# Kernel tuning notes

Hardware: AMD Instinct MI355X
Metric: run time of the kernel (lower is better)

## Reference

```python
import jax, jax.numpy as jnp
import numpy as np

B, L, D = 128, 64, 1024  # batch, tokens, encoder_size
T = 2 * L - 1            # L shifts then L-1 reduces (full binary parse)


def setup_inputs() -> dict:
    key = jax.random.key(0)
    k1, k2, k3, k4 = jax.random.split(key, 4)
    sequence = jax.random.normal(k1, (B, L, 2 * D), dtype=jnp.float32)
    # valid SPINN transition sequence: shift all tokens, then reduce to one node
    transitions = jnp.concatenate(
        [jnp.ones((B, L), jnp.int32), jnp.full((B, L - 1), 2, jnp.int32)], axis=1)
    scale = 0.02
    Ul_w = jax.random.normal(k2, (D, 5 * D), dtype=jnp.float32) * scale  # U_l weight (x @ W)
    Ul_b = jax.random.normal(k3, (5 * D,), dtype=jnp.float32) * scale    # U_l bias
    Ur_w = jax.random.normal(k4, (D, 5 * D), dtype=jnp.float32) * scale  # U_r weight (no bias)
    return {"sequence": sequence, "transitions": transitions,
            "Ul_w": Ul_w, "Ul_b": Ul_b, "Ur_w": Ur_w}


def reference(sequence, transitions, Ul_w, Ul_b, Ur_w):
    b, l, d2 = sequence.shape
    d = d2 // 2
    seq_h, seq_c = sequence[..., :d], sequence[..., d:]
    S = l + 2  # max stack depth: 2 initial copies + l shifts
    batch = jnp.arange(b)

    # stack initialized with two copies of the first buffer token (buffer NOT popped)
    stack_h = jnp.zeros((b, S, d), seq_h.dtype).at[:, 0].set(seq_h[:, 0]).at[:, 1].set(seq_h[:, 0])
    stack_c = jnp.zeros((b, S, d), seq_c.dtype).at[:, 0].set(seq_c[:, 0]).at[:, 1].set(seq_c[:, 0])
    sp = jnp.full((b,), 2, jnp.int32)   # stack pointer (next free slot)
    bp = jnp.zeros((b,), jnp.int32)     # buffer pointer (next token to shift)

    def step(carry, trans):
        stack_h, stack_c, sp, bp = carry
        is_shift = trans == 1
        is_reduce = trans == 2
        # top-2 of stack: right = top, left = second
        h_r = stack_h[batch, sp - 1]
        c_r = stack_c[batch, sp - 1]
        h_l = stack_h[batch, sp - 2]
        c_l = stack_c[batch, sp - 2]
        # TreeLSTM composition (tracking input x is None)
        gates = h_l @ Ul_w + Ul_b + h_r @ Ur_w  # (b, 5d)
        i_j, o_j, f_l, f_r, u_j = jnp.split(gates, 5, axis=1)
        c_j = (jax.nn.sigmoid(i_j) * jnp.tanh(u_j)
               + jax.nn.sigmoid(f_l) * c_l + jax.nn.sigmoid(f_r) * c_r)
        h_j = jax.nn.sigmoid(o_j) * jnp.tanh(c_j)
        # buffer head for shift
        buf_h = seq_h[batch, bp]
        buf_c = seq_c[batch, bp]
        # single conditional scatter: shift writes at sp, reduce overwrites sp-2
        widx = jnp.where(is_shift, sp, sp - 2)
        cur_h = stack_h[batch, widx]
        cur_c = stack_c[batch, widx]
        sm = is_shift[:, None]
        rm = is_reduce[:, None]
        new_h = jnp.where(sm, buf_h, jnp.where(rm, h_j, cur_h))
        new_c = jnp.where(sm, buf_c, jnp.where(rm, c_j, cur_c))
        stack_h = stack_h.at[batch, widx].set(new_h)
        stack_c = stack_c.at[batch, widx].set(new_c)
        sp = sp + jnp.where(is_shift, 1, jnp.where(is_reduce, -1, 0)).astype(sp.dtype)
        bp = bp + is_shift.astype(bp.dtype)
        return (stack_h, stack_c, sp, bp), None

    (stack_h, _, sp, _), _ = jax.lax.scan(step, (stack_h, stack_c, sp, bp), transitions.T)
    return stack_h[batch, sp - 1]  # (B, D) final hidden state on top of each stack
```

## Files before the change

kernel.cpp:

```cpp
#include <hip/hip_runtime.h>
#include <hip/hip_bf16.h>


#define ND 5120
#define NSTEP 63
#define RHS (128 * 1024)
#define NBLK2 256

typedef __attribute__((ext_vector_type(8))) short bf16x8;
typedef __attribute__((ext_vector_type(4))) float f32x4;
typedef unsigned short u16;
typedef unsigned int u32;

__device__ __forceinline__ float bf2f(u16 x) {
  unsigned int u = ((unsigned int)x) << 16;
  return __builtin_bit_cast(float, u);
}
__device__ __forceinline__ u16 f2bf(float f) {
  unsigned int u = __builtin_bit_cast(unsigned int, f);
  unsigned int lsb = (u >> 16) & 1u;
  u += 0x7fffu + lsb;
  return (u16)(u >> 16);
}
__device__ __forceinline__ void gld16(const void* g, void* l) {
  __builtin_amdgcn_global_load_lds((const __attribute__((address_space(1))) void*)g,
                                   (__attribute__((address_space(3))) void*)l, 16, 0, 0);
}

__global__ void transpose_cast_kernel(const float* __restrict__ W, u16* __restrict__ WT) {
  __shared__ float tile[64][65];
  int bid = blockIdx.x;
  int kt = bid & 15, nt = bid >> 4;
  int tid = threadIdx.x;
#pragma unroll
  for (int i = 0; i < 16; ++i) {
    int idx = i * 256 + tid;
    int r = idx >> 6, c = idx & 63;
    tile[r][c] = W[(long)(kt * 64 + r) * ND + nt * 64 + c];
  }
  __syncthreads();
#pragma unroll
  for (int i = 0; i < 16; ++i) {
    int idx = i * 256 + tid;
    int r = idx >> 6, c = idx & 63;
    WT[(long)(nt * 64 + r) * 1024 + kt * 64 + c] = f2bf(tile[c][r]);
  }
}

__global__ void prep_misc_kernel(const float* __restrict__ seq, u16* __restrict__ Xh,
                                 u16* __restrict__ RH0, float* __restrict__ RC0,
                                 int* __restrict__ bar) {
  long t = (long)blockIdx.x * 256 + threadIdx.x;
  int idx = (int)(t >> 17);
  int rem = (int)(t & 131071);
  int b = rem >> 10;
  int k = rem & 1023;
  float h = seq[((long)b * 64 + idx) * 2048 + k];
  Xh[t] = f2bf(h);
  if (idx == 63) {
    RH0[rem] = f2bf(h);
    RC0[rem] = seq[((long)b * 64 + 63) * 2048 + 1024 + k];
  }
  if (t < 2048) bar[t] = 0;
}

__launch_bounds__(256)
__global__ void phase1_kernel(const u16* __restrict__ Xh, const u16* __restrict__ WlT,
                              const float* __restrict__ Ulb, u16* __restrict__ GL) {
  __shared__ u16 As[128 * 32];
  __shared__ u16 Bs[128 * 32];
  int bid = blockIdx.x;
  int mi = bid & 63, ni = bid >> 6;
  int t = threadIdx.x;
  int w = t >> 6, lane = t & 63;
  int r16 = lane & 15, quad = lane >> 4;
  int wm = w & 1, wn = w >> 1;
  const long arow0 = (long)mi * 128;
  const long brow0 = (long)ni * 128;
  int srow = 16 * w + (lane >> 2);
  int skoff = (lane & 3) * 8;

  f32x4 acc[4][4];
#pragma unroll
  for (int a = 0; a < 4; ++a)
#pragma unroll
    for (int b = 0; b < 4; ++b) acc[a][b] = (f32x4){0.f, 0.f, 0.f, 0.f};

  for (int ks = 0; ks < 32; ++ks) {
    long k0 = (long)ks * 32 + skoff;
    gld16(Xh + (arow0 + srow) * 1024 + k0,        As + w * 512);
    gld16(Xh + (arow0 + 64 + srow) * 1024 + k0,   As + 2048 + w * 512);
    gld16(WlT + (brow0 + srow) * 1024 + k0,       Bs + w * 512);
    gld16(WlT + (brow0 + 64 + srow) * 1024 + k0,  Bs + 2048 + w * 512);
    __syncthreads();
    bf16x8 af[4], bf[4];
#pragma unroll
    for (int mt = 0; mt < 4; ++mt)
      af[mt] = *(const bf16x8*)(As + (wm * 64 + mt * 16 + r16) * 32 + quad * 8);
#pragma unroll
    for (int nt = 0; nt < 4; ++nt)
      bf[nt] = *(const bf16x8*)(Bs + (wn * 64 + nt * 16 + r16) * 32 + quad * 8);
#pragma unroll
    for (int mt = 0; mt < 4; ++mt)
#pragma unroll
      for (int nt = 0; nt < 4; ++nt)
        acc[mt][nt] = __builtin_amdgcn_mfma_f32_16x16x32_bf16(af[mt], bf[nt], acc[mt][nt], 0, 0, 0);
    __syncthreads();
  }
#pragma unroll
  for (int mt = 0; mt < 4; ++mt)
#pragma unroll
    for (int nt = 0; nt < 4; ++nt)
#pragma unroll
      for (int r = 0; r < 4; ++r) {
        long row = arow0 + wm * 64 + mt * 16 + quad * 4 + r;
        long col = brow0 + wn * 64 + nt * 16 + r16;
        GL[row * ND + col] = f2bf(acc[mt][nt][r] + Ulb[col]);
      }
}

__device__ __forceinline__ void group_barrier(int* __restrict__ bar, int grp, int cg) {
  __syncthreads();
  if (threadIdx.x == 0) {
    asm volatile("s_waitcnt vmcnt(0)" ::: "memory");
    int* base = bar + grp * 320;
    int* gen = base + 9 * 32;
    int g0 = __hip_atomic_load(gen, __ATOMIC_RELAXED, __HIP_MEMORY_SCOPE_AGENT);
    int sub = cg & 7;
    int a = __hip_atomic_fetch_add(base + sub * 32, 1, __ATOMIC_RELAXED, __HIP_MEMORY_SCOPE_AGENT);
    if (a == 7) {
      __hip_atomic_fetch_add(base + sub * 32, -8, __ATOMIC_RELAXED, __HIP_MEMORY_SCOPE_AGENT);
      int m = __hip_atomic_fetch_add(base + 8 * 32, 1, __ATOMIC_RELAXED, __HIP_MEMORY_SCOPE_AGENT);
      if (m == 7) {
        __hip_atomic_fetch_add(base + 8 * 32, -8, __ATOMIC_RELAXED, __HIP_MEMORY_SCOPE_AGENT);
        __hip_atomic_fetch_add(gen, 1, __ATOMIC_RELAXED, __HIP_MEMORY_SCOPE_AGENT);
      } else {
        while (__hip_atomic_load(gen, __ATOMIC_RELAXED, __HIP_MEMORY_SCOPE_AGENT) == g0)
          __builtin_amdgcn_s_sleep(2);
      }
    } else {
      while (__hip_atomic_load(gen, __ATOMIC_RELAXED, __HIP_MEMORY_SCOPE_AGENT) == g0)
        __builtin_amdgcn_s_sleep(2);
    }
    __atomic_signal_fence(__ATOMIC_ACQUIRE);
  }
  __syncthreads();
}

__launch_bounds__(512, 1)
__global__ void phase2_kernel(const float* __restrict__ seq, const u16* __restrict__ WrT,
                              const u16* __restrict__ GL, const u16* __restrict__ RH0,
                              u16* __restrict__ Xring, const float* __restrict__ RC0,
                              int* __restrict__ bar, float* __restrict__ out) {
  __shared__ float plds[4][5][32][18];
  int bid = blockIdx.x;
  int rhf = bid & 3, cg = bid >> 2;
  int tid = threadIdx.x;
  int wv = tid >> 6, lane = tid & 63;
  int r16 = lane & 15, quad = lane >> 4;
  int mt = wv & 1, kq = wv >> 1;
  int col = cg * 16 + r16;
  int rowA = rhf * 32 + mt * 16;
  int kbase = kq * 256 + quad * 8;

  bf16x8 bw[5][8];
#pragma unroll
  for (int g = 0; g < 5; ++g)
#pragma unroll
    for (int ks = 0; ks < 8; ++ks)
      bw[g][ks] = *(const bf16x8*)(WrT + (long)(g * 1024 + col) * 1024 + kbase + ks * 32);
#pragma unroll
  for (int g = 0; g < 5; ++g)
#pragma unroll
    for (int ks = 0; ks < 8; ++ks)
      asm volatile("" : "+v"(bw[g][ks]));

  const long aoff = (long)(rowA + r16) * 1024 + kbase;

  int act = tid < 256;
  int row_l = tid >> 3, cp = tid & 7;
  int erow = rhf * 32 + row_l;
  int ecol0 = cg * 16 + cp * 2;
  float c0 = 0.f, c1 = 0.f;
  if (act) {
    c0 = RC0[(long)erow * 1024 + ecol0];
    c1 = RC0[(long)erow * 1024 + ecol0 + 1];
  }

  for (int j = 1; j <= NSTEP; ++j) {
    const u16* rhbuf = (j == 1) ? RH0 : (Xring + (long)(j - 2) * RHS);
    int idx = 63 - j;

    bf16x8 af[8];
#pragma unroll
    for (int ks = 0; ks < 8; ++ks)
      af[ks] = *(const bf16x8*)(rhbuf + aoff + ks * 32);
    u32 pgl[5];
    float2 pcl = {0.f, 0.f};
    if (act) {
      long glb = ((long)idx * 128 + erow) * ND + ecol0;
#pragma unroll
      for (int g = 0; g < 5; ++g)
        pgl[g] = *(const u32*)(GL + glb + g * 1024);
      pcl = *(const float2*)(seq + ((long)erow * 64 + idx) * 2048 + 1024 + ecol0);
    }

    f32x4 acc[5];
#pragma unroll
    for (int g = 0; g < 5; ++g) acc[g] = (f32x4){0.f, 0.f, 0.f, 0.f};
#pragma unroll
    for (int ks = 0; ks < 8; ++ks)
#pragma unroll
      for (int g = 0; g < 5; ++g)
        acc[g] = __builtin_amdgcn_mfma_f32_16x16x32_bf16(af[ks], bw[g][ks], acc[g], 0, 0, 0);

#pragma unroll
    for (int g = 0; g < 5; ++g)
#pragma unroll
      for (int r = 0; r < 4; ++r)
        plds[kq][g][mt * 16 + quad * 4 + r][r16] = acc[g][r];
    __syncthreads();

    if (act) {
      float h0, h1;
#pragma unroll
      for (int c = 0; c < 2; ++c) {
        int cl = cp * 2 + c;
        float gg[5];
#pragma unroll
        for (int g = 0; g < 5; ++g)
          gg[g] = plds[0][g][row_l][cl] + plds[1][g][row_l][cl] +
                  plds[2][g][row_l][cl] + plds[3][g][row_l][cl];
        u16 glo = (c == 0) ? 0 : 0;
        float gi  = gg[0] + bf2f((u16)((c ? pgl[0] >> 16 : pgl[0]) & 0xffff));
        float go  = gg[1] + bf2f((u16)((c ? pgl[1] >> 16 : pgl[1]) & 0xffff));
        float gfl = gg[2] + bf2f((u16)((c ? pgl[2] >> 16 : pgl[2]) & 0xffff));
        float gfr = gg[3] + bf2f((u16)((c ? pgl[3] >> 16 : pgl[3]) & 0xffff));
        float gu  = gg[4] + bf2f((u16)((c ? pgl[4] >> 16 : pgl[4]) & 0xffff));
        float c_l = c ? pcl.y : pcl.x;
        float c_r = c ? c1 : c0;
        float si  = 1.f / (1.f + __expf(-gi));
        float so  = 1.f / (1.f + __expf(-go));
        float sfl = 1.f / (1.f + __expf(-gfl));
        float sfr = 1.f / (1.f + __expf(-gfr));
        float cj = si * tanhf(gu) + sfl * c_l + sfr * c_r;
        float hj = so * tanhf(cj);
        if (c == 0) { c0 = cj; h0 = hj; } else { c1 = cj; h1 = hj; }
        (void)glo;
      }
      if (j < NSTEP) {
        u32 hv = (u32)f2bf(h0) | ((u32)f2bf(h1) << 16);
        u32* dst = (u32*)Xring + (long)(j - 1) * (RHS / 2) + erow * 512 + cg * 8 + cp;
        __hip_atomic_store(dst, hv, __ATOMIC_RELAXED, __HIP_MEMORY_SCOPE_AGENT);
      } else {
        float2 o2 = {h0, h1};
        *(float2*)(out + (long)erow * 1024 + ecol0) = o2;
      }
    }
    if (j < NSTEP) group_barrier(bar, rhf, cg);
  }
}

extern "C" void kernel_launch(void* const* d_in, const int* in_sizes, int n_in,
                              void* d_out, int out_size, void* d_ws, size_t ws_size,
                              hipStream_t stream) {
  const float* seq = (const float*)d_in[0];
  const float* Ulw = (const float*)d_in[2];
  const float* Ulb = (const float*)d_in[3];
  const float* Urw = (const float*)d_in[4];
  float* out = (float*)d_out;

  char* p = (char*)d_ws;
  u16* WlT = (u16*)p;  p += 10485760;
  u16* WrT = (u16*)p;  p += 10485760;
  u16* Xh  = (u16*)p;  p += 16777216;
  u16* GL  = (u16*)p;  p += 83886080;
  u16* RH0 = (u16*)p;  p += 524288;
  float* RC0 = (float*)p; p += 1048576;
  int* bar = (int*)p;  p += 8192;

  hipLaunchKernelGGL(transpose_cast_kernel, dim3(1280), dim3(256), 0, stream, Ulw, WlT);
  hipLaunchKernelGGL(transpose_cast_kernel, dim3(1280), dim3(256), 0, stream, Urw, WrT);
  hipLaunchKernelGGL(prep_misc_kernel, dim3(32768), dim3(256), 0, stream, seq, Xh, RH0, RC0, bar);
  hipLaunchKernelGGL(phase1_kernel, dim3(2560), dim3(256), 0, stream, Xh, WlT, Ulb, GL);
  hipLaunchKernelGGL(phase2_kernel, dim3(NBLK2), dim3(512), 0, stream,
                     seq, WrT, GL, RH0, Xh, RC0, bar, out);
}
```

Measured before the change: 566.9 us.

## Replace group barrier with per-wave readiness flags in recurrent phase

Removes the hierarchical atomic group barrier between recurrence steps. Each producing wave now publishes a flag once its hidden-state slice is stored, and each consumer wave spins only on the flags covering its own K-slice of the next step's input. The goal is to cut barrier latency and let waves run ahead as soon as their inputs are ready. In exchange, the per-step __syncthreads that protected shared-memory partials from being overwritten is gone, so there is a possible intra-block race. A bounded spin loop that can exit on timeout also risks silently reading stale data.

```diff
diff --git a/kernel.cpp b/kernel.cpp
--- a/kernel.cpp
+++ b/kernel.cpp
@@ -49,7 +49,7 @@
 
 __global__ void prep_misc_kernel(const float* __restrict__ seq, u16* __restrict__ Xh,
                                  u16* __restrict__ RH0, float* __restrict__ RC0,
-                                 int* __restrict__ bar) {
+                                 int* __restrict__ flags) {
   long t = (long)blockIdx.x * 256 + threadIdx.x;
   int idx = (int)(t >> 17);
   int rem = (int)(t & 131071);
@@ -61,7 +61,7 @@
     RH0[rem] = f2bf(h);
     RC0[rem] = seq[((long)b * 64 + 63) * 2048 + 1024 + k];
   }
-  if (t < 2048) bar[t] = 0;
+  if (t < 63488) flags[t] = 0;
 }
 
 __launch_bounds__(256)
@@ -119,39 +119,11 @@
       }
 }
 
-__device__ __forceinline__ void group_barrier(int* __restrict__ bar, int grp, int cg) {
-  __syncthreads();
-  if (threadIdx.x == 0) {
-    asm volatile("s_waitcnt vmcnt(0)" ::: "memory");
-    int* base = bar + grp * 320;
-    int* gen = base + 9 * 32;
-    int g0 = __hip_atomic_load(gen, __ATOMIC_RELAXED, __HIP_MEMORY_SCOPE_AGENT);
-    int sub = cg & 7;
-    int a = __hip_atomic_fetch_add(base + sub * 32, 1, __ATOMIC_RELAXED, __HIP_MEMORY_SCOPE_AGENT);
-    if (a == 7) {
-      __hip_atomic_fetch_add(base + sub * 32, -8, __ATOMIC_RELAXED, __HIP_MEMORY_SCOPE_AGENT);
-      int m = __hip_atomic_fetch_add(base + 8 * 32, 1, __ATOMIC_RELAXED, __HIP_MEMORY_SCOPE_AGENT);
-      if (m == 7) {
-        __hip_atomic_fetch_add(base + 8 * 32, -8, __ATOMIC_RELAXED, __HIP_MEMORY_SCOPE_AGENT);
-        __hip_atomic_fetch_add(gen, 1, __ATOMIC_RELAXED, __HIP_MEMORY_SCOPE_AGENT);
-      } else {
-        while (__hip_atomic_load(gen, __ATOMIC_RELAXED, __HIP_MEMORY_SCOPE_AGENT) == g0)
-          __builtin_amdgcn_s_sleep(2);
-      }
-    } else {
-      while (__hip_atomic_load(gen, __ATOMIC_RELAXED, __HIP_MEMORY_SCOPE_AGENT) == g0)
-        __builtin_amdgcn_s_sleep(2);
-    }
-    __atomic_signal_fence(__ATOMIC_ACQUIRE);
-  }
-  __syncthreads();
-}
-
 __launch_bounds__(512, 1)
 __global__ void phase2_kernel(const float* __restrict__ seq, const u16* __restrict__ WrT,
                               const u16* __restrict__ GL, const u16* __restrict__ RH0,
                               u16* __restrict__ Xring, const float* __restrict__ RC0,
-                              int* __restrict__ bar, float* __restrict__ out) {
+                              int* __restrict__ flags, float* __restrict__ out) {
   __shared__ float plds[4][5][32][18];
   int bid = blockIdx.x;
   int rhf = bid & 3, cg = bid >> 2;
@@ -187,14 +159,11 @@
     c1 = RC0[(long)erow * 1024 + ecol0 + 1];
   }
 
+  int* const gflags = flags;
+
   for (int j = 1; j <= NSTEP; ++j) {
-    const u16* rhbuf = (j == 1) ? RH0 : (Xring + (long)(j - 2) * RHS);
-    int idx = 63 - j;
-
-    bf16x8 af[8];
-#pragma unroll
-    for (int ks = 0; ks < 8; ++ks)
-      af[ks] = *(const bf16x8*)(rhbuf + aoff + ks * 32);
+    const int idx = 63 - j;
+
     u32 pgl[5];
     float2 pcl = {0.f, 0.f};
     if (act) {
@@ -205,6 +174,24 @@
       pcl = *(const float2*)(seq + ((long)erow * 64 + idx) * 2048 + 1024 + ecol0);
     }
 
+    if (j >= 2) {
+      const int fbase = ((rhf * 62 + (j - 2)) * 64 + kq * 16) * 4 + lane;
+      int spin = 0;
+      for (;;) {
+        int v = __hip_atomic_load(gflags + fbase, __ATOMIC_RELAXED, __HIP_MEMORY_SCOPE_AGENT);
+        if (__all(v != 0)) break;
+        if (++spin > (1 << 17)) break;
+        __builtin_amdgcn_s_sleep(1);
+      }
+      asm volatile("" ::: "memory");
+    }
+
+    const u16* rhbuf = (j == 1) ? RH0 : (Xring + (long)(j - 2) * RHS);
+    bf16x8 af[8];
+#pragma unroll
+    for (int ks = 0; ks < 8; ++ks)
+      af[ks] = *(const bf16x8*)(rhbuf + aoff + ks * 32);
+
     f32x4 acc[5];
 #pragma unroll
     for (int g = 0; g < 5; ++g) acc[g] = (f32x4){0.f, 0.f, 0.f, 0.f};
@@ -222,7 +209,7 @@
     __syncthreads();
 
     if (act) {
-      float h0, h1;
+      float h0 = 0.f, h1 = 0.f;
 #pragma unroll
       for (int c = 0; c < 2; ++c) {
         int cl = cp * 2 + c;
@@ -231,7 +218,6 @@
         for (int g = 0; g < 5; ++g)
           gg[g] = plds[0][g][row_l][cl] + plds[1][g][row_l][cl] +
                   plds[2][g][row_l][cl] + plds[3][g][row_l][cl];
-        u16 glo = (c == 0) ? 0 : 0;
         float gi  = gg[0] + bf2f((u16)((c ? pgl[0] >> 16 : pgl[0]) & 0xffff));
         float go  = gg[1] + bf2f((u16)((c ? pgl[1] >> 16 : pgl[1]) & 0xffff));
         float gfl = gg[2] + bf2f((u16)((c ? pgl[2] >> 16 : pgl[2]) & 0xffff));
@@ -246,18 +232,21 @@
         float cj = si * tanhf(gu) + sfl * c_l + sfr * c_r;
         float hj = so * tanhf(cj);
         if (c == 0) { c0 = cj; h0 = hj; } else { c1 = cj; h1 = hj; }
-        (void)glo;
       }
       if (j < NSTEP) {
         u32 hv = (u32)f2bf(h0) | ((u32)f2bf(h1) << 16);
         u32* dst = (u32*)Xring + (long)(j - 1) * (RHS / 2) + erow * 512 + cg * 8 + cp;
         __hip_atomic_store(dst, hv, __ATOMIC_RELAXED, __HIP_MEMORY_SCOPE_AGENT);
+        asm volatile("s_waitcnt vmcnt(0)" ::: "memory");
+        if (lane == 0) {
+          int fidx = ((rhf * 62 + (j - 1)) * 64 + cg) * 4 + wv;
+          __hip_atomic_store(gflags + fidx, 1, __ATOMIC_RELAXED, __HIP_MEMORY_SCOPE_AGENT);
+        }
       } else {
         float2 o2 = {h0, h1};
         *(float2*)(out + (long)erow * 1024 + ecol0) = o2;
       }
     }
-    if (j < NSTEP) group_barrier(bar, rhf, cg);
   }
 }
 
@@ -276,13 +265,14 @@
   u16* Xh  = (u16*)p;  p += 16777216;
   u16* GL  = (u16*)p;  p += 83886080;
   u16* RH0 = (u16*)p;  p += 524288;
-  float* RC0 = (float*)p; p += 1048576;
-  int* bar = (int*)p;  p += 8192;
+  float* RC0 = (float*)p;
+  int* flags = (int*)(p + 524288);
+  p += 1048576;
 
   hipLaunchKernelGGL(transpose_cast_kernel, dim3(1280), dim3(256), 0, stream, Ulw, WlT);
   hipLaunchKernelGGL(transpose_cast_kernel, dim3(1280), dim3(256), 0, stream, Urw, WrT);
-  hipLaunchKernelGGL(prep_misc_kernel, dim3(32768), dim3(256), 0, stream, seq, Xh, RH0, RC0, bar);
+  hipLaunchKernelGGL(prep_misc_kernel, dim3(32768), dim3(256), 0, stream, seq, Xh, RH0, RC0, flags);
   hipLaunchKernelGGL(phase1_kernel, dim3(2560), dim3(256), 0, stream, Xh, WlT, Ulb, GL);
   hipLaunchKernelGGL(phase2_kernel, dim3(NBLK2), dim3(512), 0, stream,
-                     seq, WrT, GL, RH0, Xh, RC0, bar, out);
-}
+                     seq, WrT, GL, RH0, Xh, RC0, flags, out);
+}
```

New measurement: 819.0 us. 1.44x slower.
